# Kernel optimization log

Hardware: AMD Instinct MI355X
Metric: run time of the kernel (lower is better)

The kernel has to match this reference:

```python
import jax, jax.numpy as jnp
import numpy as np

B, T, C = 4, 2048, 1024
H = 16
D = C // H  # head_dim = 64


def setup_inputs() -> dict:
    key = jax.random.key(0)
    k1, k2, k3 = jax.random.split(key, 3)
    x = jax.random.normal(k1, (B, T, C), dtype=jnp.float32)
    w_qkv = jax.random.normal(k2, (3 * C, C), dtype=jnp.float32) * (1.0 / np.sqrt(C))
    w_proj = jax.random.normal(k3, (C, C), dtype=jnp.float32) * (1.0 / np.sqrt(C))
    return {"x": x, "w_qkv": w_qkv, "w_proj": w_proj}


def reference(x, w_qkv, w_proj):
    Bx, Tx, Cx = x.shape
    qkv = jnp.einsum('btc,fc->btf', x, w_qkv)  # [B,T,3C]
    q, k, v = jnp.split(qkv, 3, axis=-1)
    # [B,H,T,D]
    q = q.reshape(Bx, Tx, H, D).transpose(0, 2, 1, 3)
    k = k.reshape(Bx, Tx, H, D).transpose(0, 2, 1, 3)
    v = v.reshape(Bx, Tx, H, D).transpose(0, 2, 1, 3)
    scale = 1.0 / np.sqrt(D)
    scores = jnp.einsum('bhqd,bhkd->bhqk', q, k) * scale
    causal = jnp.tril(jnp.ones((Tx, Tx), dtype=bool))
    scores = jnp.where(causal, scores, jnp.finfo(scores.dtype).min)
    attn = jax.nn.softmax(scores, axis=-1)
    out = jnp.einsum('bhqk,bhkd->bhqd', attn, v)  # [B,H,T,D]
    out = out.transpose(0, 2, 1, 3).reshape(Bx, Tx, Cx)
    return jnp.einsum('btc,oc->bto', out, w_proj)
```

## Files before the change

kernel.cpp:

```cpp
#include <hip/hip_runtime.h>
#include <hip/hip_bf16.h>
#include <stdint.h>

#define Bx 4
#define Tx 2048
#define Cx 1024
#define Hx 16
#define Dx 64
#define Mx (Bx*Tx)

typedef __bf16 bf16x8 __attribute__((ext_vector_type(8)));
typedef float f32x4 __attribute__((ext_vector_type(4)));
typedef unsigned short u16x8 __attribute__((ext_vector_type(8)));

__device__ __forceinline__ unsigned short f2bf(float f) {
  union { float f; unsigned u; } v; v.f = f;
  unsigned r = v.u + 0x7fffu + ((v.u >> 16) & 1u);
  return (unsigned short)(r >> 16);
}

__global__ void cvt_kernel(const float* __restrict__ in, unsigned short* __restrict__ out, int n) {
  int i = blockIdx.x * blockDim.x + threadIdx.x;
  int idx = i << 3;
  if (idx >= n) return;
  const float4* p = (const float4*)(in + idx);
  float4 a = p[0], b = p[1];
  u16x8 o;
  o[0] = f2bf(a.x); o[1] = f2bf(a.y); o[2] = f2bf(a.z); o[3] = f2bf(a.w);
  o[4] = f2bf(b.x); o[5] = f2bf(b.y); o[6] = f2bf(b.z); o[7] = f2bf(b.w);
  *(u16x8*)(out + idx) = o;
}

#define GLOAD_LDS16(g, l) \
  __builtin_amdgcn_global_load_lds((const __attribute__((address_space(1))) void*)(g), \
                                   (__attribute__((address_space(3))) void*)(l), 16, 0, 0)

template<int OUT_F32>
__global__ __launch_bounds__(512, 1) void gemm8p(const unsigned short* __restrict__ A,
                                                 const unsigned short* __restrict__ Bm,
                                                 void* __restrict__ Cv,
                                                 int M, int N, int K)
{
  __shared__ unsigned short As[2][256 * 64];
  __shared__ unsigned short Bs[2][128 * 64];
  const int tid = threadIdx.x;
  const int wave = tid >> 6, lane = tid & 63;
  const int l15 = lane & 15, l4 = lane >> 4;
  const int wm = wave >> 1, wn = wave & 1;
  const int NB = N >> 7;
  const int cpx = (int)gridDim.x >> 3;
  const int bid = (int)blockIdx.x;
  const int swz = (bid & 7) * cpx + (bid >> 3);
  const int bx = swz % NB, by = swz / NB;
  const int mBase = by << 8, nBase = bx << 7;

  const int srow   = tid >> 3;
  const int schunk = (tid & 7) ^ (srow & 7);
  const unsigned short* aSrc = A  + (size_t)(mBase + srow) * K + (schunk << 3);
  const unsigned short* bSrc = Bm + (size_t)(nBase + srow) * K + (schunk << 3);
  const int dstOff = wave << 9;

  f32x4 acc[4][4];
  #pragma unroll
  for (int i = 0; i < 4; ++i)
    #pragma unroll
    for (int j = 0; j < 4; ++j) { acc[i][j][0]=0.f; acc[i][j][1]=0.f; acc[i][j][2]=0.f; acc[i][j][3]=0.f; }

  const int NT = K >> 6;
  const int s7 = l15 & 7;

#define STAGE6(k0, buf) do { \
    GLOAD_LDS16(aSrc + (k0),                   &As[buf][dstOff]); \
    GLOAD_LDS16(aSrc + (size_t) 64*K + (k0),   &As[buf][ 4096 + dstOff]); \
    GLOAD_LDS16(aSrc + (size_t)128*K + (k0),   &As[buf][ 8192 + dstOff]); \
    GLOAD_LDS16(aSrc + (size_t)192*K + (k0),   &As[buf][12288 + dstOff]); \
    GLOAD_LDS16(bSrc + (k0),                   &Bs[buf][dstOff]); \
    GLOAD_LDS16(bSrc + (size_t) 64*K + (k0),   &Bs[buf][ 4096 + dstOff]); \
  } while (0)

  STAGE6(0, 0);
  for (int t = 0; t < NT; ++t) {
    const int buf = t & 1;
    if (t + 1 < NT) {
      STAGE6((t + 1) << 6, buf ^ 1);
      asm volatile("s_waitcnt vmcnt(6)" ::: "memory");
    } else {
      asm volatile("s_waitcnt vmcnt(0)" ::: "memory");
    }
    __builtin_amdgcn_s_barrier();
    asm volatile("" ::: "memory");

    const unsigned short* curA = As[buf];
    const unsigned short* curB = Bs[buf];
    #pragma unroll
    for (int kk = 0; kk < 2; ++kk) {
      const int ch = ((kk << 2) | l4) ^ s7;
      bf16x8 af[4], bfr[4];
      #pragma unroll
      for (int mi = 0; mi < 4; ++mi)
        af[mi]  = *(const bf16x8*)&curA[((wm << 6) + (mi << 4) + l15) * 64 + (ch << 3)];
      #pragma unroll
      for (int nj = 0; nj < 4; ++nj)
        bfr[nj] = *(const bf16x8*)&curB[((wn << 6) + (nj << 4) + l15) * 64 + (ch << 3)];
      __builtin_amdgcn_s_setprio(1);
      #pragma unroll
      for (int mi = 0; mi < 4; ++mi)
        #pragma unroll
        for (int nj = 0; nj < 4; ++nj)
          acc[mi][nj] = __builtin_amdgcn_mfma_f32_16x16x32_bf16(af[mi], bfr[nj], acc[mi][nj], 0, 0, 0);
      __builtin_amdgcn_s_setprio(0);
    }
    asm volatile("" ::: "memory");
    __builtin_amdgcn_s_barrier();
  }
#undef STAGE6

  #pragma unroll
  for (int mi = 0; mi < 4; ++mi)
    #pragma unroll
    for (int nj = 0; nj < 4; ++nj) {
      const int row = mBase + (wm << 6) + (mi << 4) + (l4 << 2);
      const int col = nBase + (wn << 6) + (nj << 4) + l15;
      #pragma unroll
      for (int r = 0; r < 4; ++r) {
        float v = acc[mi][nj][r];
        if (OUT_F32) ((float*)Cv)[(size_t)(row + r) * N + col] = v;
        else ((unsigned short*)Cv)[(size_t)(row + r) * N + col] = f2bf(v);
      }
    }
}

__global__ void vtrans_kernel(const unsigned short* __restrict__ qkv, unsigned short* __restrict__ vt) {
  const int bh = blockIdx.y;
  const int b = bh >> 4, h = bh & 15;
  const int t0 = blockIdx.x << 6;
  __shared__ unsigned short tile[64][65];
  const int tid = threadIdx.x;
  const unsigned short* src = qkv + (size_t)b * Tx * 3072 + 2048 + h * 64;
  for (int e = tid; e < 4096; e += 256) {
    int r = e >> 6, c = e & 63;
    tile[c][r] = src[(size_t)(t0 + r) * 3072 + c];
  }
  __syncthreads();
  unsigned short* dst = vt + (size_t)bh * 64 * Tx + t0;
  for (int e = tid; e < 4096; e += 256) {
    int d = e >> 6, tt = e & 63;
    dst[(size_t)d * Tx + tt] = tile[d][tt];
  }
}

__device__ __forceinline__ void compute_half(
    const unsigned short* __restrict__ Ks, const unsigned short* __restrict__ Vs,
    unsigned short* __restrict__ Plw,
    bf16x8 aq0, bf16x8 aq1, float* m_run, float* rs, f32x4* oacc,
    int qrow0, int kv0, bool diag, int l15, int l4)
{
  const float SC = 0.125f * 1.44269504f;
  f32x4 s[4];
  #pragma unroll
  for (int nt = 0; nt < 4; ++nt) { s[nt][0]=0.f; s[nt][1]=0.f; s[nt][2]=0.f; s[nt][3]=0.f; }
  #pragma unroll
  for (int nt = 0; nt < 4; ++nt) {
    const int r = (nt << 4) + l15, sz = r & 7;
    bf16x8 bk0 = *(const bf16x8*)&Ks[r * 64 + ((l4 ^ sz) << 3)];
    bf16x8 bk1 = *(const bf16x8*)&Ks[r * 64 + (((l4 + 4) ^ sz) << 3)];
    s[nt] = __builtin_amdgcn_mfma_f32_16x16x32_bf16(aq0, bk0, s[nt], 0, 0, 0);
    s[nt] = __builtin_amdgcn_mfma_f32_16x16x32_bf16(aq1, bk1, s[nt], 0, 0, 0);
  }
  #pragma unroll
  for (int nt = 0; nt < 4; ++nt) {
    const int kv = kv0 + (nt << 4) + l15;
    #pragma unroll
    for (int r = 0; r < 4; ++r) {
      float val = s[nt][r] * SC;
      if (diag && kv > qrow0 + (l4 << 2) + r) val = -3.0e38f;
      s[nt][r] = val;
    }
  }
  float pm[4];
  #pragma unroll
  for (int r = 0; r < 4; ++r)
    pm[r] = fmaxf(fmaxf(s[0][r], s[1][r]), fmaxf(s[2][r], s[3][r]));
  int ok = (pm[0] <= m_run[0] + 8.f) & (pm[1] <= m_run[1] + 8.f)
         & (pm[2] <= m_run[2] + 8.f) & (pm[3] <= m_run[3] + 8.f);
  if (!__all(ok)) {
    #pragma unroll
    for (int off = 1; off < 16; off <<= 1)
      #pragma unroll
      for (int r = 0; r < 4; ++r) pm[r] = fmaxf(pm[r], __shfl_xor(pm[r], off));
    #pragma unroll
    for (int r = 0; r < 4; ++r) {
      float mnew = fmaxf(m_run[r], pm[r]);
      float corr = exp2f(m_run[r] - mnew);
      rs[r] *= corr;
      #pragma unroll
      for (int nt = 0; nt < 4; ++nt) oacc[nt][r] *= corr;
      m_run[r] = mnew;
    }
  }
  #pragma unroll
  for (int nt = 0; nt < 4; ++nt)
    #pragma unroll
    for (int r = 0; r < 4; ++r) {
      float p = exp2f(s[nt][r] - m_run[r]);
      s[nt][r] = p;
      rs[r] += p;
    }
  #pragma unroll
  for (int nt = 0; nt < 4; ++nt)
    #pragma unroll
    for (int r = 0; r < 4; ++r)
      Plw[((l4 << 2) + r) * 72 + (nt << 4) + l15] = f2bf(s[nt][r]);
  asm volatile("s_waitcnt lgkmcnt(0)" ::: "memory");
  __builtin_amdgcn_sched_barrier(0);
  bf16x8 ap0 = *(const bf16x8*)&Plw[l15 * 72 + (l4 << 3)];
  bf16x8 ap1 = *(const bf16x8*)&Plw[l15 * 72 + 32 + (l4 << 3)];
  #pragma unroll
  for (int nt = 0; nt < 4; ++nt) {
    const int r = (nt << 4) + l15, vz = r & 7;
    bf16x8 bv0 = *(const bf16x8*)&Vs[r * 64 + ((l4 ^ vz) << 3)];
    bf16x8 bv1 = *(const bf16x8*)&Vs[r * 64 + (((l4 + 4) ^ vz) << 3)];
    oacc[nt] = __builtin_amdgcn_mfma_f32_16x16x32_bf16(ap0, bv0, oacc[nt], 0, 0, 0);
    oacc[nt] = __builtin_amdgcn_mfma_f32_16x16x32_bf16(ap1, bv1, oacc[nt], 0, 0, 0);
  }
}

__global__ __launch_bounds__(256, 4) void attn_kernel(const unsigned short* __restrict__ qkv,
                                                      const unsigned short* __restrict__ vt,
                                                      unsigned short* __restrict__ aout)
{
  const int id = blockIdx.x;
  const int xcd = id & 7, sblk = id >> 3;
  const int xblk = sblk & 15;
  const int bh = (xcd << 3) + (sblk >> 4);
  const int b = bh >> 4, h = bh & 15;
  const int wave = threadIdx.x >> 6, lane = threadIdx.x & 63;
  const int l15 = lane & 15, l4 = lane >> 4;
  const int qi0 = (xblk << 2) + wave;

  const unsigned short* qp = qkv + (size_t)b * Tx * 3072 + h * 64;
  const unsigned short* kp = qp + 1024;
  const unsigned short* vp = vt + (size_t)bh * 64 * Tx;
  unsigned short* op = aout + (size_t)b * Tx * 1024 + h * 64;

  __shared__ unsigned short Ks[64 * 64];
  __shared__ unsigned short Vs[64 * 64];
  __shared__ unsigned short Pl[4][2][16 * 72];

  const int qiA = qi0, qiB = 127 - qi0;
  const int qrA = qiA << 4, qrB = qiB << 4;
  const int lastA = xblk, lastB = 31 - xblk;

  bf16x8 aqA0 = *(const bf16x8*)&qp[(size_t)(qrA + l15) * 3072 + (l4 << 3)];
  bf16x8 aqA1 = *(const bf16x8*)&qp[(size_t)(qrA + l15) * 3072 + 32 + (l4 << 3)];
  bf16x8 aqB0 = *(const bf16x8*)&qp[(size_t)(qrB + l15) * 3072 + (l4 << 3)];
  bf16x8 aqB1 = *(const bf16x8*)&qp[(size_t)(qrB + l15) * 3072 + 32 + (l4 << 3)];

  float mA[4], rsA[4], mB[4], rsB[4];
  f32x4 oA[4], oB[4];
  #pragma unroll
  for (int r = 0; r < 4; ++r) { mA[r]=0.f; rsA[r]=0.f; mB[r]=0.f; rsB[r]=0.f; }
  #pragma unroll
  for (int nt = 0; nt < 4; ++nt) {
    oA[nt][0]=0.f; oA[nt][1]=0.f; oA[nt][2]=0.f; oA[nt][3]=0.f;
    oB[nt][0]=0.f; oB[nt][1]=0.f; oB[nt][2]=0.f; oB[nt][3]=0.f;
  }

  const int srw = lane >> 3;
  const int sj  = (lane & 7) ^ srw;

  for (int kvt = 0; kvt <= lastB; ++kvt) {
    const int kv0 = kvt << 6;
    {
      const int c0 = wave << 1, c1 = c0 + 1;
      const int r0 = (c0 << 3) + srw, r1 = (c1 << 3) + srw;
      GLOAD_LDS16(kp + (size_t)(kv0 + r0) * 3072 + (sj << 3), Ks + (c0 << 9));
      GLOAD_LDS16(kp + (size_t)(kv0 + r1) * 3072 + (sj << 3), Ks + (c1 << 9));
      GLOAD_LDS16(vp + (size_t)r0 * 2048 + kv0 + (sj << 3),   Vs + (c0 << 9));
      GLOAD_LDS16(vp + (size_t)r1 * 2048 + kv0 + (sj << 3),   Vs + (c1 << 9));
    }
    __syncthreads();

    compute_half(Ks, Vs, Pl[wave][1], aqB0, aqB1, mB, rsB, oB, qrB, kv0, kvt == lastB, l15, l4);
    if (kvt <= lastA)
      compute_half(Ks, Vs, Pl[wave][0], aqA0, aqA1, mA, rsA, oA, qrA, kv0, kvt == lastA, l15, l4);

    __syncthreads();
  }

  #pragma unroll
  for (int off = 1; off < 16; off <<= 1)
    #pragma unroll
    for (int r = 0; r < 4; ++r) { rsA[r] += __shfl_xor(rsA[r], off); rsB[r] += __shfl_xor(rsB[r], off); }
  #pragma unroll
  for (int r = 0; r < 4; ++r) {
    const float invA = 1.0f / rsA[r], invB = 1.0f / rsB[r];
    #pragma unroll
    for (int nt = 0; nt < 4; ++nt) {
      op[(size_t)(qrA + (l4 << 2) + r) * 1024 + (nt << 4) + l15] = f2bf(oA[nt][r] * invA);
      op[(size_t)(qrB + (l4 << 2) + r) * 1024 + (nt << 4) + l15] = f2bf(oB[nt][r] * invB);
    }
  }
}

extern "C" void kernel_launch(void* const* d_in, const int* in_sizes, int n_in,
                              void* d_out, int out_size, void* d_ws, size_t ws_size,
                              hipStream_t stream) {
  const float* x     = (const float*)d_in[0];
  const float* wqkv  = (const float*)d_in[1];
  const float* wproj = (const float*)d_in[2];

  char* ws = (char*)d_ws;
  unsigned short* qkvb = (unsigned short*)(ws);
  unsigned short* vtb  = (unsigned short*)(ws + 50331648);
  unsigned short* xb   = (unsigned short*)(ws + 50331648 + 16777216);
  unsigned short* wqb  = (unsigned short*)(ws + 50331648 + 16777216 + 16777216);
  unsigned short* wpb  = (unsigned short*)(ws + 50331648 + 16777216 + 16777216 + 6291456);
  unsigned short* aob  = xb;

  cvt_kernel<<<4096, 256, 0, stream>>>(x,     xb,  Bx * Tx * Cx);
  cvt_kernel<<<1536, 256, 0, stream>>>(wqkv,  wqb, 3 * Cx * Cx);
  cvt_kernel<<<512,  256, 0, stream>>>(wproj, wpb, Cx * Cx);

  gemm8p<0><<<dim3(768), 512, 0, stream>>>(xb, wqb, qkvb, Mx, 3072, 1024);
  vtrans_kernel<<<dim3(32, 64), 256, 0, stream>>>(qkvb, vtb);
  attn_kernel<<<1024, 256, 0, stream>>>(qkvb, vtb, aob);
  gemm8p<1><<<dim3(256), 512, 0, stream>>>(aob, wpb, d_out, Mx, 1024, 1024);
}
```

Measured before the change: 298.9 us.

## Triple-buffer GEMM LDS staging and interleave loads with MFMA halves

The GEMM moves from a double-buffered to a triple-buffered LDS pipeline with prefetch distance two. Global-to-LDS loads for tile t+2 are split into two groups placed between the two k-halves of MFMA work, and the trailing barrier per iteration is removed. The goal is to hide global latency better and cut barrier overhead. In exchange, LDS use rises to 144KB per block, and dropping the trailing barrier depends on the three-buffer rotation to avoid write-after-read hazards.

```diff
diff --git a/kernel.cpp b/kernel.cpp
--- a/kernel.cpp
+++ b/kernel.cpp
@@ -41,8 +41,8 @@
                                                  void* __restrict__ Cv,
                                                  int M, int N, int K)
 {
-  __shared__ unsigned short As[2][256 * 64];
-  __shared__ unsigned short Bs[2][128 * 64];
+  __shared__ unsigned short As[3][256 * 64];
+  __shared__ unsigned short Bs[3][128 * 64];
   const int tid = threadIdx.x;
   const int wave = tid >> 6, lane = tid & 63;
   const int l15 = lane & 15, l4 = lane >> 4;
@@ -69,32 +69,32 @@
   const int NT = K >> 6;
   const int s7 = l15 & 7;
 
-#define STAGE6(k0, buf) do { \
-    GLOAD_LDS16(aSrc + (k0),                   &As[buf][dstOff]); \
-    GLOAD_LDS16(aSrc + (size_t) 64*K + (k0),   &As[buf][ 4096 + dstOff]); \
-    GLOAD_LDS16(aSrc + (size_t)128*K + (k0),   &As[buf][ 8192 + dstOff]); \
-    GLOAD_LDS16(aSrc + (size_t)192*K + (k0),   &As[buf][12288 + dstOff]); \
-    GLOAD_LDS16(bSrc + (k0),                   &Bs[buf][dstOff]); \
-    GLOAD_LDS16(bSrc + (size_t) 64*K + (k0),   &Bs[buf][ 4096 + dstOff]); \
-  } while (0)
-
-  STAGE6(0, 0);
+#define STG_A(k0, dst, j)  GLOAD_LDS16(aSrc + (size_t)(64*(j))*K + (k0), (dst) + 4096*(j) + dstOff)
+#define STG_B(k0, dst, j)  GLOAD_LDS16(bSrc + (size_t)(64*(j))*K + (k0), (dst) + 4096*(j) + dstOff)
+
+  STG_A(0, As[0], 0); STG_A(0, As[0], 1); STG_A(0, As[0], 2); STG_A(0, As[0], 3);
+  STG_B(0, Bs[0], 0); STG_B(0, Bs[0], 1);
+  STG_A(64, As[1], 0); STG_A(64, As[1], 1); STG_A(64, As[1], 2); STG_A(64, As[1], 3);
+  STG_B(64, Bs[1], 0); STG_B(64, Bs[1], 1);
+
+  int bufR = 0;
   for (int t = 0; t < NT; ++t) {
-    const int buf = t & 1;
-    if (t + 1 < NT) {
-      STAGE6((t + 1) << 6, buf ^ 1);
-      asm volatile("s_waitcnt vmcnt(6)" ::: "memory");
-    } else {
-      asm volatile("s_waitcnt vmcnt(0)" ::: "memory");
-    }
+    if (t + 1 < NT) asm volatile("s_waitcnt vmcnt(6)" ::: "memory");
+    else            asm volatile("s_waitcnt vmcnt(0)" ::: "memory");
     __builtin_amdgcn_s_barrier();
     asm volatile("" ::: "memory");
 
-    const unsigned short* curA = As[buf];
-    const unsigned short* curB = Bs[buf];
-    #pragma unroll
-    for (int kk = 0; kk < 2; ++kk) {
-      const int ch = ((kk << 2) | l4) ^ s7;
+    const unsigned short* curA = As[bufR];
+    const unsigned short* curB = Bs[bufR];
+    int bufS = bufR + 2; if (bufS >= 3) bufS -= 3;
+    unsigned short* sA = As[bufS];
+    unsigned short* sB = Bs[bufS];
+    const bool doStage = (t + 2 < NT);
+    const int k2 = (t + 2) << 6;
+
+    if (doStage) { STG_A(k2, sA, 0); STG_A(k2, sA, 1); STG_A(k2, sA, 2); }
+    {
+      const int ch = l4 ^ s7;
       bf16x8 af[4], bfr[4];
       #pragma unroll
       for (int mi = 0; mi < 4; ++mi)
@@ -110,10 +110,29 @@
           acc[mi][nj] = __builtin_amdgcn_mfma_f32_16x16x32_bf16(af[mi], bfr[nj], acc[mi][nj], 0, 0, 0);
       __builtin_amdgcn_s_setprio(0);
     }
+    if (doStage) { STG_A(k2, sA, 3); STG_B(k2, sB, 0); STG_B(k2, sB, 1); }
+    {
+      const int ch = (4 | l4) ^ s7;
+      bf16x8 af[4], bfr[4];
+      #pragma unroll
+      for (int mi = 0; mi < 4; ++mi)
+        af[mi]  = *(const bf16x8*)&curA[((wm << 6) + (mi << 4) + l15) * 64 + (ch << 3)];
+      #pragma unroll
+      for (int nj = 0; nj < 4; ++nj)
+        bfr[nj] = *(const bf16x8*)&curB[((wn << 6) + (nj << 4) + l15) * 64 + (ch << 3)];
+      __builtin_amdgcn_s_setprio(1);
+      #pragma unroll
+      for (int mi = 0; mi < 4; ++mi)
+        #pragma unroll
+        for (int nj = 0; nj < 4; ++nj)
+          acc[mi][nj] = __builtin_amdgcn_mfma_f32_16x16x32_bf16(af[mi], bfr[nj], acc[mi][nj], 0, 0, 0);
+      __builtin_amdgcn_s_setprio(0);
+    }
     asm volatile("" ::: "memory");
-    __builtin_amdgcn_s_barrier();
-  }
-#undef STAGE6
+    bufR = (bufR == 2) ? 0 : bufR + 1;
+  }
+#undef STG_A
+#undef STG_B
 
   #pragma unroll
   for (int mi = 0; mi < 4; ++mi)
```

Measured after the change: 309.4 us. +3.5%, slower.
